# Kernel optimization log

Measured on AMD Instinct MI355X. Metric: run time of the kernel, lower is better.

The kernel has to match this reference:

```python
import jax, jax.numpy as jnp
import numpy as np

N_SEGMENTS = 196  # matches init kwarg n_segments

def setup_inputs() -> dict:
    key = jax.random.key(0)
    k1, k2, k3 = jax.random.split(key, 3)
    B, C, H, W_img = 8, 3, 224, 224
    img = jax.random.normal(k1, (B, C, H, W_img), dtype=jnp.float32)
    segments = jax.random.randint(k2, (B, H, W_img), 0, N_SEGMENTS)
    W = jax.random.normal(k3, (C + 2, 768), dtype=jnp.float32) * 0.02
    b = jnp.zeros((768,), dtype=jnp.float32)
    return {"img": img, "segments": segments, "W": W, "b": b}

def reference(img, segments, W, b):
    B, C, H, W_img = img.shape
    N = H * W_img
    E = W.shape[1]
    # [B, N, C]
    img_flat = img.reshape(B, C, N).transpose(0, 2, 1)
    # normalized coords: torch meshgrid(y/(H-1), x/(W-1), indexing='ij'), stacked as (x, y)
    y = (jnp.arange(H, dtype=jnp.float32) / (H - 1))[:, None]          # [H,1]
    x = (jnp.arange(W_img, dtype=jnp.float32) / (W_img - 1))[None, :]  # [1,W]
    xg = jnp.broadcast_to(x, (H, W_img))
    yg = jnp.broadcast_to(y, (H, W_img))
    coords = jnp.stack((xg, yg), axis=-1).reshape(1, N, 2)             # [1,N,2]
    coords = jnp.broadcast_to(coords, (B, N, 2))
    feat = jnp.concatenate([img_flat, coords], axis=-1)                # [B,N,C+2]
    # linear projection per pixel
    pix = jnp.einsum('bnf,fe->bne', feat, W) + b                       # [B,N,E]
    # per-batch offset segment ids
    seg_ids = segments.reshape(B, N) + jnp.arange(B)[:, None] * N_SEGMENTS
    seg_ids = seg_ids.reshape(B * N)
    sums = jax.ops.segment_sum(pix.reshape(B * N, E), seg_ids,
                               num_segments=B * N_SEGMENTS)
    counts = jax.ops.segment_sum(jnp.ones((B * N,), dtype=pix.dtype), seg_ids,
                                 num_segments=B * N_SEGMENTS)
    # scatter_mean semantics: empty segments yield 0 (sum is 0, guard divide)
    out = sums / jnp.maximum(counts, 1.0)[:, None]
    return out.reshape(B, N_SEGMENTS, E)
```

## Files before the change

### kernel.cpp

```cpp
#include <hip/hip_runtime.h>

#define NSEG 196
#define BATCH 8
#define IMH 224
#define IMW 224
#define NPIX (IMH * IMW)
#define EMB 768
#define ACC_STRIDE 6

#define CHUNKS_PER_BATCH 64

__global__ __launch_bounds__(256)
void spt_accum_kernel(const float* __restrict__ img,
                      const int* __restrict__ seg,
                      float* __restrict__ ws) {
    __shared__ float lacc[NSEG * ACC_STRIDE];

    const int tid = threadIdx.x;
    for (int i = tid; i < NSEG * ACC_STRIDE; i += 256) lacc[i] = 0.0f;
    __syncthreads();

    const int batch = blockIdx.x / CHUNKS_PER_BATCH;
    const int chunk = blockIdx.x % CHUNKS_PER_BATCH;
    const int pix_per_chunk = (NPIX + CHUNKS_PER_BATCH - 1) / CHUNKS_PER_BATCH;
    const int n0 = chunk * pix_per_chunk;
    const int n1 = (n0 + pix_per_chunk < NPIX) ? (n0 + pix_per_chunk) : NPIX;

    const float* __restrict__ imgb = img + (size_t)batch * 3 * NPIX;
    const int*   __restrict__ segb = seg + (size_t)batch * NPIX;

    const float inv223 = 1.0f / 223.0f;

    for (int n = n0 + tid; n < n1; n += 256) {
        const float c0 = imgb[n];
        const float c1 = imgb[NPIX + n];
        const float c2 = imgb[2 * NPIX + n];
        const int   s  = segb[n];
        const int   h  = n / IMW;
        const int   w  = n - h * IMW;
        const float x  = (float)w * inv223;
        const float y  = (float)h * inv223;
        float* p = &lacc[s * ACC_STRIDE];
        atomicAdd(&p[0], c0);
        atomicAdd(&p[1], c1);
        atomicAdd(&p[2], c2);
        atomicAdd(&p[3], x);
        atomicAdd(&p[4], y);
        atomicAdd(&p[5], 1.0f);
    }
    __syncthreads();

    float* __restrict__ wsb = ws + (size_t)batch * NSEG * ACC_STRIDE;
    for (int i = tid; i < NSEG * ACC_STRIDE; i += 256) {
        const float v = lacc[i];
        if (v != 0.0f) atomicAdd(&wsb[i], v);
    }
}

__global__ __launch_bounds__(256)
void spt_project_kernel(const float* __restrict__ ws,
                        const float* __restrict__ Wm,
                        const float* __restrict__ bias,
                        float* __restrict__ out) {
    const int bs = blockIdx.x;
    __shared__ float fs[ACC_STRIDE];
    if (threadIdx.x < ACC_STRIDE) fs[threadIdx.x] = ws[bs * ACC_STRIDE + threadIdx.x];
    __syncthreads();

    const float cnt = fs[5];
    const float inv = 1.0f / fmaxf(cnt, 1.0f);
    const float f0 = fs[0], f1 = fs[1], f2 = fs[2], f3 = fs[3], f4 = fs[4];

    float* __restrict__ outb = out + (size_t)bs * EMB;
    #pragma unroll
    for (int it = 0; it < 3; ++it) {
        const int e = threadIdx.x + it * 256;
        float acc = cnt * bias[e];
        acc += f0 * Wm[0 * EMB + e];
        acc += f1 * Wm[1 * EMB + e];
        acc += f2 * Wm[2 * EMB + e];
        acc += f3 * Wm[3 * EMB + e];
        acc += f4 * Wm[4 * EMB + e];
        outb[e] = acc * inv;
    }
}

extern "C" void kernel_launch(void* const* d_in, const int* in_sizes, int n_in,
                              void* d_out, int out_size, void* d_ws, size_t ws_size,
                              hipStream_t stream) {
    const float* img  = (const float*)d_in[0];
    const int*   seg  = (const int*)d_in[1];
    const float* Wm   = (const float*)d_in[2];
    const float* bias = (const float*)d_in[3];
    float* out = (float*)d_out;
    float* ws  = (float*)d_ws;

    hipMemsetAsync(ws, 0, (size_t)BATCH * NSEG * ACC_STRIDE * sizeof(float), stream);

    spt_accum_kernel<<<BATCH * CHUNKS_PER_BATCH, 256, 0, stream>>>(img, seg, ws);
    spt_project_kernel<<<BATCH * NSEG, 256, 0, stream>>>(ws, Wm, bias, out);
}
```

Baseline: 80.07 us.

## Replace global atomics with per-block partials and replicated LDS histograms

The accumulate kernel now uses 8 replicated shared-memory histograms to cut LDS atomic contention. Each block handles a fixed 512-pixel chunk with vectorized float2/int2 loads and writes its partial sums to its own workspace slice instead of issuing global atomics. The projection kernel reduces the 98 partials per batch with a wave shuffle, which removes the memset launch and the global atomics. In exchange there is more shared-memory zeroing per block, a larger workspace, and extra reads in the projection stage.

```diff
diff --git a/kernel.cpp b/kernel.cpp
--- a/kernel.cpp
+++ b/kernel.cpp
@@ -6,81 +6,112 @@
 #define IMW 224
 #define NPIX (IMH * IMW)
 #define EMB 768
-#define ACC_STRIDE 6
-
-#define CHUNKS_PER_BATCH 64
+#define ST 6
+#define SEGSZ (NSEG * ST)
+#define NCOPY 8
+#define CHUNK 512
+#define CPB (NPIX / CHUNK)
+#define NBLK1 (BATCH * CPB)
 
 __global__ __launch_bounds__(256)
-void spt_accum_kernel(const float* __restrict__ img,
-                      const int* __restrict__ seg,
-                      float* __restrict__ ws) {
-    __shared__ float lacc[NSEG * ACC_STRIDE];
-
+void spt_accum(const float* __restrict__ img, const int* __restrict__ seg,
+               float* __restrict__ ws) {
+    __shared__ float lacc[NCOPY][SEGSZ];
     const int tid = threadIdx.x;
-    for (int i = tid; i < NSEG * ACC_STRIDE; i += 256) lacc[i] = 0.0f;
+    for (int i = tid; i < NCOPY * SEGSZ; i += 256) (&lacc[0][0])[i] = 0.0f;
     __syncthreads();
 
-    const int batch = blockIdx.x / CHUNKS_PER_BATCH;
-    const int chunk = blockIdx.x % CHUNKS_PER_BATCH;
-    const int pix_per_chunk = (NPIX + CHUNKS_PER_BATCH - 1) / CHUNKS_PER_BATCH;
-    const int n0 = chunk * pix_per_chunk;
-    const int n1 = (n0 + pix_per_chunk < NPIX) ? (n0 + pix_per_chunk) : NPIX;
+    const int batch = blockIdx.x / CPB;
+    const int chunk = blockIdx.x % CPB;
+    const int n = chunk * CHUNK + tid * 2;
 
-    const float* __restrict__ imgb = img + (size_t)batch * 3 * NPIX;
-    const int*   __restrict__ segb = seg + (size_t)batch * NPIX;
+    const float* imgb = img + (size_t)batch * 3 * NPIX;
+    const float2 c0 = *(const float2*)(imgb + n);
+    const float2 c1 = *(const float2*)(imgb + NPIX + n);
+    const float2 c2 = *(const float2*)(imgb + 2 * NPIX + n);
+    const int2   s2 = *(const int2*)(seg + (size_t)batch * NPIX + n);
 
-    const float inv223 = 1.0f / 223.0f;
+    const int h  = n / IMW;
+    const int wb = n - h * IMW;
+    const float y = (float)h * (1.0f / 223.0f);
+    float* lc = &lacc[tid & (NCOPY - 1)][0];
 
-    for (int n = n0 + tid; n < n1; n += 256) {
-        const float c0 = imgb[n];
-        const float c1 = imgb[NPIX + n];
-        const float c2 = imgb[2 * NPIX + n];
-        const int   s  = segb[n];
-        const int   h  = n / IMW;
-        const int   w  = n - h * IMW;
-        const float x  = (float)w * inv223;
-        const float y  = (float)h * inv223;
-        float* p = &lacc[s * ACC_STRIDE];
-        atomicAdd(&p[0], c0);
-        atomicAdd(&p[1], c1);
-        atomicAdd(&p[2], c2);
-        atomicAdd(&p[3], x);
-        atomicAdd(&p[4], y);
-        atomicAdd(&p[5], 1.0f);
+    {
+        float* p = lc + s2.x * ST;
+        atomicAdd(p + 0, c0.x);
+        atomicAdd(p + 1, c1.x);
+        atomicAdd(p + 2, c2.x);
+        atomicAdd(p + 3, (float)wb * (1.0f / 223.0f));
+        atomicAdd(p + 4, y);
+        atomicAdd(p + 5, 1.0f);
+    }
+    {
+        float* p = lc + s2.y * ST;
+        atomicAdd(p + 0, c0.y);
+        atomicAdd(p + 1, c1.y);
+        atomicAdd(p + 2, c2.y);
+        atomicAdd(p + 3, (float)(wb + 1) * (1.0f / 223.0f));
+        atomicAdd(p + 4, y);
+        atomicAdd(p + 5, 1.0f);
     }
     __syncthreads();
 
-    float* __restrict__ wsb = ws + (size_t)batch * NSEG * ACC_STRIDE;
-    for (int i = tid; i < NSEG * ACC_STRIDE; i += 256) {
-        const float v = lacc[i];
-        if (v != 0.0f) atomicAdd(&wsb[i], v);
+    float* wsb = ws + (size_t)blockIdx.x * SEGSZ;
+    for (int i = tid; i < SEGSZ; i += 256) {
+        float v = lacc[0][i];
+        #pragma unroll
+        for (int c = 1; c < NCOPY; ++c) v += lacc[c][i];
+        wsb[i] = v;
     }
 }
 
 __global__ __launch_bounds__(256)
-void spt_project_kernel(const float* __restrict__ ws,
-                        const float* __restrict__ Wm,
-                        const float* __restrict__ bias,
-                        float* __restrict__ out) {
+void spt_proj(const float* __restrict__ ws, const float* __restrict__ Wm,
+              const float* __restrict__ bias, float* __restrict__ out) {
     const int bs = blockIdx.x;
-    __shared__ float fs[ACC_STRIDE];
-    if (threadIdx.x < ACC_STRIDE) fs[threadIdx.x] = ws[bs * ACC_STRIDE + threadIdx.x];
+    const int batch = bs / NSEG;
+    const int s = bs - batch * NSEG;
+    __shared__ float fs[ST];
+    const int tid = threadIdx.x;
+
+    if (tid < 64) {
+        float v0 = 0, v1 = 0, v2 = 0, v3 = 0, v4 = 0, v5 = 0;
+        const float* base = ws + (size_t)batch * CPB * SEGSZ + s * ST;
+        for (int c = tid; c < CPB; c += 64) {
+            const float* p = base + (size_t)c * SEGSZ;
+            v0 += p[0]; v1 += p[1]; v2 += p[2];
+            v3 += p[3]; v4 += p[4]; v5 += p[5];
+        }
+        #pragma unroll
+        for (int off = 32; off > 0; off >>= 1) {
+            v0 += __shfl_xor(v0, off, 64);
+            v1 += __shfl_xor(v1, off, 64);
+            v2 += __shfl_xor(v2, off, 64);
+            v3 += __shfl_xor(v3, off, 64);
+            v4 += __shfl_xor(v4, off, 64);
+            v5 += __shfl_xor(v5, off, 64);
+        }
+        if (tid == 0) {
+            fs[0] = v0; fs[1] = v1; fs[2] = v2;
+            fs[3] = v3; fs[4] = v4; fs[5] = v5;
+        }
+    }
     __syncthreads();
 
     const float cnt = fs[5];
     const float inv = 1.0f / fmaxf(cnt, 1.0f);
     const float f0 = fs[0], f1 = fs[1], f2 = fs[2], f3 = fs[3], f4 = fs[4];
 
-    float* __restrict__ outb = out + (size_t)bs * EMB;
+    float* outb = out + (size_t)bs * EMB;
     #pragma unroll
     for (int it = 0; it < 3; ++it) {
-        const int e = threadIdx.x + it * 256;
+        const int e = tid + it * 256;
         float acc = cnt * bias[e];
-        acc += f0 * Wm[0 * EMB + e];
-        acc += f1 * Wm[1 * EMB + e];
-        acc += f2 * Wm[2 * EMB + e];
-        acc += f3 * Wm[3 * EMB + e];
-        acc += f4 * Wm[4 * EMB + e];
+        acc = fmaf(f0, Wm[0 * EMB + e], acc);
+        acc = fmaf(f1, Wm[1 * EMB + e], acc);
+        acc = fmaf(f2, Wm[2 * EMB + e], acc);
+        acc = fmaf(f3, Wm[3 * EMB + e], acc);
+        acc = fmaf(f4, Wm[4 * EMB + e], acc);
         outb[e] = acc * inv;
     }
 }
@@ -95,8 +126,6 @@
     float* out = (float*)d_out;
     float* ws  = (float*)d_ws;
 
-    hipMemsetAsync(ws, 0, (size_t)BATCH * NSEG * ACC_STRIDE * sizeof(float), stream);
-
-    spt_accum_kernel<<<BATCH * CHUNKS_PER_BATCH, 256, 0, stream>>>(img, seg, ws);
-    spt_project_kernel<<<BATCH * NSEG, 256, 0, stream>>>(ws, Wm, bias, out);
+    spt_accum<<<NBLK1, 256, 0, stream>>>(img, seg, ws);
+    spt_proj<<<BATCH * NSEG, 256, 0, stream>>>(ws, Wm, bias, out);
 }
```

Measured after the change: 86.92 us. 8.6% more time.
